# Kernel optimization log

Measured on AMD Instinct MI355X. Metric: run time of the kernel, lower is better.

Reference implementation:

```python
import jax, jax.numpy as jnp
import numpy as np

N = 20000   # nodes
E = 320000  # edges (before self-loops)
D = 256     # feature width (inChl = hdChl = outChl)
H = 4       # heads
C = D // H  # per-head channels = 64
NEG_SLOPE = 0.2
LN_EPS = 1e-5


def setup_inputs() -> dict:
    key = jax.random.key(0)
    ks = jax.random.split(key, 2 + 4 * 4)
    inp = {}
    inp["x"] = jax.random.normal(ks[0], (1, N, D), dtype=jnp.float32)
    inp["edge_index"] = jax.random.randint(ks[1], (2, E), 0, N, dtype=jnp.int32)
    s = 1.0 / np.sqrt(D)
    for i in range(4):
        k = 2 + 4 * i
        inp[f"Wl{i+1}"] = (jax.random.normal(ks[k], (D, H * C), dtype=jnp.float32) * s)
        inp[f"Wr{i+1}"] = (jax.random.normal(ks[k + 1], (D, H * C), dtype=jnp.float32) * s)
        inp[f"att{i+1}"] = (jax.random.normal(ks[k + 2], (H, C), dtype=jnp.float32) * s)
        inp[f"b{i+1}"] = jnp.zeros((H * C,), dtype=jnp.float32)
        inp[f"g{i+1}"] = jnp.ones((D,), dtype=jnp.float32)
        inp[f"be{i+1}"] = jnp.zeros((D,), dtype=jnp.float32)
    return inp


def _segment_softmax(scores, seg, num_segments):
    # scores: [E, H], per-destination softmax over incoming edges
    m = jax.ops.segment_max(scores, seg, num_segments=num_segments)
    e = jnp.exp(scores - m[seg])
    d = jax.ops.segment_sum(e, seg, num_segments=num_segments)
    return e / d[seg]


def _gatv2(x, src, dst, Wl, Wr, att, b):
    # GATv2Conv defaults: share_weights=False, concat=True, negative_slope=0.2
    n = x.shape[0]
    xl = (x @ Wl).reshape(n, H, C)  # source transform
    xr = (x @ Wr).reshape(n, H, C)  # target transform
    m = xl[src] + xr[dst]                                  # [E', H, C]
    e = jnp.sum(jax.nn.leaky_relu(m, NEG_SLOPE) * att, -1) # [E', H]
    alpha = _segment_softmax(e, dst, n)                    # [E', H]
    out = jax.ops.segment_sum(xl[src] * alpha[:, :, None], dst, num_segments=n)
    return out.reshape(n, H * C) + b


def _layernorm(x, g, b):
    mu = jnp.mean(x, -1, keepdims=True)
    var = jnp.mean(jnp.square(x - mu), -1, keepdims=True)
    return (x - mu) * jax.lax.rsqrt(var + LN_EPS) * g + b


def _forward(x, edge_index, layers):
    h = x[0]  # squeeze batch dim -> [N, D]
    n = h.shape[0]
    loop = jnp.arange(n, dtype=edge_index.dtype)
    src = jnp.concatenate([edge_index[0], loop])  # add_self_loops=True
    dst = jnp.concatenate([edge_index[1], loop])
    for (Wl, Wr, att, b, g, be) in layers:
        h = _gatv2(h, src, dst, Wl, Wr, att, b)
        h = jax.nn.relu(_layernorm(h, g, be))
    return h[None]  # unsqueeze -> [1, N, D]


def reference(x, edge_index,
              Wl1, Wr1, att1, b1, g1, be1,
              Wl2, Wr2, att2, b2, g2, be2,
              Wl3, Wr3, att3, b3, g3, be3,
              Wl4, Wr4, att4, b4, g4, be4):
    layers = [(Wl1, Wr1, att1, b1, g1, be1),
              (Wl2, Wr2, att2, b2, g2, be2),
              (Wl3, Wr3, att3, b3, g3, be3),
              (Wl4, Wr4, att4, b4, g4, be4)]
    return _forward(x, edge_index, layers)
```

## Files before the change

### kernel.cpp

```cpp
#include <hip/hip_runtime.h>
#include <math.h>

#define N_NODES 20000
#define E_EDGES 320000
#define EP (E_EDGES + N_NODES)
#define D 256
#define NHEAD 4
#define CH 64
#define NEG_SLOPE 0.2f
#define LN_EPS 1e-5f

typedef _Float16 half8_t __attribute__((ext_vector_type(8)));
typedef _Float16 half4_t __attribute__((ext_vector_type(4)));
typedef _Float16 half2_t __attribute__((ext_vector_type(2)));
typedef float   float4_t __attribute__((ext_vector_type(4)));

__device__ __forceinline__ void async_cp16(const void* g, void* l)
{
    __builtin_amdgcn_global_load_lds(
        (const __attribute__((address_space(1))) void*)g,
        (__attribute__((address_space(3))) void*)l, 16, 0, 0);
}

template<int CTRL>
__device__ __forceinline__ float dpp_add(float v) {
    int t = __builtin_amdgcn_update_dpp(0, __float_as_int(v), CTRL, 0xF, 0xF, true);
    return v + __int_as_float(t);
}
__device__ __forceinline__ float row_sum16(float v) {
    v = dpp_add<0x121>(v);
    v = dpp_add<0x122>(v);
    v = dpp_add<0x124>(v);
    v = dpp_add<0x128>(v);
    return v;
}

__global__ __launch_bounds__(256)
void convert_x_kernel(const float* __restrict__ x, _Float16* __restrict__ h16,
                      int* __restrict__ deg)
{
    int i = blockIdx.x * 256 + threadIdx.x;
    if (i < N_NODES) deg[i] = 0;
    if (i >= N_NODES * D / 4) return;
    float4 v = reinterpret_cast<const float4*>(x)[i];
    half4_t o;
    o.x = (_Float16)v.x; o.y = (_Float16)v.y; o.z = (_Float16)v.z; o.w = (_Float16)v.w;
    reinterpret_cast<half4_t*>(h16)[i] = o;
}

__global__ __launch_bounds__(256)
void csr_hist_kernel(const int* __restrict__ ei, int* __restrict__ deg)
{
    int e = blockIdx.x * 256 + threadIdx.x;
    if (e >= EP) return;
    int dst = (e < E_EDGES) ? ei[E_EDGES + e] : (e - E_EDGES);
    atomicAdd(&deg[dst], 1);
}

__global__ __launch_bounds__(1024)
void csr_scan_kernel(const int* __restrict__ deg, int* __restrict__ rowptr,
                     int* __restrict__ cursor, int* __restrict__ csr_src)
{
    __shared__ int wsum[16];
    int t = threadIdx.x, lane = t & 63, w = t >> 6;
    if (t < 8) csr_src[EP + t] = 0;
    int base = t * 20;
    int loc[20];
    int s = 0;
    #pragma unroll
    for (int k = 0; k < 20; ++k) {
        int idx = base + k;
        loc[k] = (idx < N_NODES) ? deg[idx] : 0;
        s += loc[k];
    }
    int x = s;
    #pragma unroll
    for (int o = 1; o < 64; o <<= 1) {
        int y = __shfl_up(x, o, 64);
        if (lane >= o) x += y;
    }
    if (lane == 63) wsum[w] = x;
    __syncthreads();
    if (t == 0) {
        int sacc = 0;
        #pragma unroll
        for (int k = 0; k < 16; ++k) { int tmp = wsum[k]; wsum[k] = sacc; sacc += tmp; }
        rowptr[N_NODES] = sacc;
    }
    __syncthreads();
    int excl = wsum[w] + x - s;
    #pragma unroll
    for (int k = 0; k < 20; ++k) {
        int idx = base + k;
        if (idx < N_NODES) { rowptr[idx] = excl; cursor[idx] = excl; }
        excl += loc[k];
    }
}

__global__ __launch_bounds__(256)
void csr_scatter_kernel(const int* __restrict__ ei, int* __restrict__ cursor,
                        int* __restrict__ csr_src)
{
    int e = blockIdx.x * 256 + threadIdx.x;
    if (e >= EP) return;
    int src, dst;
    if (e < E_EDGES) { src = ei[e]; dst = ei[E_EDGES + e]; }
    else             { src = dst = e - E_EDGES; }
    int pos = atomicAdd(&cursor[dst], 1);
    csr_src[pos] = src;
}

struct WPtrs { const float* p[8]; };
__global__ __launch_bounds__(256)
void convw_all_kernel(WPtrs wp, _Float16* __restrict__ Wt_all)
{
    __shared__ float tile[64][65];
    const float* W = wp.p[blockIdx.z];
    _Float16* out = Wt_all + (size_t)blockIdx.z * 65536;
    int bx = blockIdx.x * 64, by = blockIdx.y * 64;
    int t = threadIdx.x;
    #pragma unroll
    for (int i = 0; i < 16; ++i) {
        int idx = t + i * 256;
        int kk = idx >> 6, nn = idx & 63;
        tile[kk][nn] = W[(by + kk) * 256 + bx + nn];
    }
    __syncthreads();
    #pragma unroll
    for (int i = 0; i < 16; ++i) {
        int idx = t + i * 256;
        int nn = idx >> 6, kk = idx & 63;
        out[(bx + nn) * 256 + by + kk] = (_Float16)tile[kk][nn];
    }
}

#define BM 128
#define BN 128
#define BK 64
#define EPAD 136
__global__ __launch_bounds__(256)
void gemm_f16_kernel(const _Float16* __restrict__ A16, const _Float16* __restrict__ Wt,
                     _Float16* __restrict__ X0, _Float16* __restrict__ X1, int nrows)
{
    const _Float16* W = Wt + blockIdx.z * 65536 + blockIdx.y * (BN * 256);
    _Float16* X = blockIdx.z ? X1 : X0;
    const int row0 = blockIdx.x * BM;
    const int col0 = blockIdx.y * BN;

    __shared__ __align__(1024) char smem[4 * 32 * EPAD * 2];
    _Float16 (*As)[BK] = reinterpret_cast<_Float16 (*)[BK]>(smem);
    _Float16 (*Bs)[BK] = reinterpret_cast<_Float16 (*)[BK]>(smem + BM * BK * 2);
    _Float16* As_flat = reinterpret_cast<_Float16*>(smem);
    _Float16* Bs_flat = reinterpret_cast<_Float16*>(smem + BM * BK * 2);
    _Float16* ep = reinterpret_cast<_Float16*>(smem);

    const int tid  = threadIdx.x;
    const int wave = tid >> 6, lane = tid & 63;
    const int quad = lane >> 4, l16 = lane & 15;

    float4_t acc[2][8];
    #pragma unroll
    for (int i = 0; i < 2; ++i)
        #pragma unroll
        for (int j = 0; j < 8; ++j) acc[i][j] = (float4_t)0.0f;

    const int r_in  = lane >> 3;
    const int c_in  = (lane & 7) * 8;

    #pragma unroll
    for (int k0 = 0; k0 < 256; k0 += BK) {
        #pragma unroll
        for (int j = 0; j < 4; ++j) {
            int ia  = wave * 4 + j;
            int row = ia * 8 + r_in;
            int gra = row0 + row;
            gra = (gra < nrows) ? gra : (nrows - 1);
            async_cp16(A16 + (size_t)gra * 256 + k0 + c_in, As_flat + ia * 512);
            async_cp16(W   + (size_t)row * 256 + k0 + c_in, Bs_flat + ia * 512);
        }
        __syncthreads();

        #pragma unroll
        for (int s = 0; s < 2; ++s) {
            half8_t af[2], bf[8];
            #pragma unroll
            for (int i = 0; i < 2; ++i)
                af[i] = *reinterpret_cast<const half8_t*>(&As[wave * 32 + i * 16 + l16][s * 32 + quad * 8]);
            #pragma unroll
            for (int j = 0; j < 8; ++j)
                bf[j] = *reinterpret_cast<const half8_t*>(&Bs[j * 16 + l16][s * 32 + quad * 8]);
            #pragma unroll
            for (int i = 0; i < 2; ++i)
                #pragma unroll
                for (int j = 0; j < 8; ++j)
                    acc[i][j] = __builtin_amdgcn_mfma_f32_16x16x32_f16(af[i], bf[j], acc[i][j], 0, 0, 0);
        }
        __syncthreads();
    }

    _Float16* epw = ep + wave * 32 * EPAD;
    #pragma unroll
    for (int i = 0; i < 2; ++i)
        #pragma unroll
        for (int j = 0; j < 8; ++j)
            #pragma unroll
            for (int r = 0; r < 4; ++r)
                epw[(i * 16 + quad * 4 + r) * EPAD + j * 16 + l16] = (_Float16)acc[i][j][r];
    #pragma unroll
    for (int t = 0; t < 8; ++t) {
        int row = t * 4 + quad;
        int gr = row0 + wave * 32 + row;
        half8_t v = *reinterpret_cast<const half8_t*>(&epw[row * EPAD + l16 * 8]);
        if (gr < nrows)
            *reinterpret_cast<half8_t*>(X + gr * 256 + col0 + l16 * 8) = v;
    }
}

__global__ __launch_bounds__(256)
void gat_fused_kernel(const _Float16* __restrict__ xl, const _Float16* __restrict__ xr,
                      const int* __restrict__ rowptr, const int* __restrict__ csr_src,
                      const float* __restrict__ att,
                      const float* __restrict__ bias, const float* __restrict__ g,
                      const float* __restrict__ be,
                      float* __restrict__ out32, _Float16* __restrict__ out16,
                      int write32)
{
    const int tid = threadIdx.x;
    const int w = tid >> 6, lane = tid & 63;
    const int n = blockIdx.x * 4 + w;
    const int start = rowptr[n], end = rowptr[n + 1];
    const int c0 = lane * 4;

    half2_t xr01, xr23, att01, att23;
    {
        half4_t xh = *reinterpret_cast<const half4_t*>(xr + n * D + c0);
        xr01.x = xh.x; xr01.y = xh.y; xr23.x = xh.z; xr23.y = xh.w;
        float4 av = *reinterpret_cast<const float4*>(att + c0);
        att01.x = (_Float16)av.x; att01.y = (_Float16)av.y;
        att23.x = (_Float16)av.z; att23.y = (_Float16)av.w;
    }
    const half2_t k02 = {(_Float16)NEG_SLOPE, (_Float16)NEG_SLOPE};

    float den = 0.0f;
    float4 num = make_float4(0.0f, 0.0f, 0.0f, 0.0f);

    int i = start;
    for (; i + 8 <= end; i += 8) {
        int sidx[8];
        #pragma unroll
        for (int j = 0; j < 8; ++j) sidx[j] = csr_src[i + j];
        half4_t h[8];
        #pragma unroll
        for (int j = 0; j < 8; ++j)
            h[j] = *reinterpret_cast<const half4_t*>(xl + sidx[j] * D + c0);
        float p[8];
        #pragma unroll
        for (int j = 0; j < 8; ++j) {
            half2_t a01 = {h[j].x, h[j].y}, a23 = {h[j].z, h[j].w};
            half2_t t0 = a01 + xr01, t1 = a23 + xr23;
            t0 = __builtin_elementwise_max(t0, t0 * k02);
            t1 = __builtin_elementwise_max(t1, t1 * k02);
            float v = __builtin_amdgcn_fdot2(t0, att01, 0.0f, false);
            p[j]    = __builtin_amdgcn_fdot2(t1, att23, v,   false);
        }
        #pragma unroll
        for (int j = 0; j < 8; ++j) p[j] = row_sum16(p[j]);
        #pragma unroll
        for (int j = 0; j < 8; ++j) p[j] = __expf(p[j]);
        #pragma unroll
        for (int j = 0; j < 8; ++j) {
            den += p[j];
            num.x = fmaf(p[j], (float)h[j].x, num.x);
            num.y = fmaf(p[j], (float)h[j].y, num.y);
            num.z = fmaf(p[j], (float)h[j].z, num.z);
            num.w = fmaf(p[j], (float)h[j].w, num.w);
        }
    }
    for (; i < end; i += 4) {
        int sidx[4];
        #pragma unroll
        for (int j = 0; j < 4; ++j) sidx[j] = csr_src[i + j];
        half4_t h[4];
        #pragma unroll
        for (int j = 0; j < 4; ++j)
            h[j] = *reinterpret_cast<const half4_t*>(xl + sidx[j] * D + c0);
        float p[4];
        #pragma unroll
        for (int j = 0; j < 4; ++j) {
            half2_t a01 = {h[j].x, h[j].y}, a23 = {h[j].z, h[j].w};
            half2_t t0 = a01 + xr01, t1 = a23 + xr23;
            t0 = __builtin_elementwise_max(t0, t0 * k02);
            t1 = __builtin_elementwise_max(t1, t1 * k02);
            float v = __builtin_amdgcn_fdot2(t0, att01, 0.0f, false);
            p[j]    = __builtin_amdgcn_fdot2(t1, att23, v,   false);
        }
        #pragma unroll
        for (int j = 0; j < 4; ++j) p[j] = row_sum16(p[j]);
        #pragma unroll
        for (int j = 0; j < 4; ++j) {
            float pj = (i + j < end) ? __expf(p[j]) : 0.0f;
            den += pj;
            num.x = fmaf(pj, (float)h[j].x, num.x);
            num.y = fmaf(pj, (float)h[j].y, num.y);
            num.z = fmaf(pj, (float)h[j].z, num.z);
            num.w = fmaf(pj, (float)h[j].w, num.w);
        }
    }

    float inv_den = 1.0f / den;
    float4 bi = *reinterpret_cast<const float4*>(bias + c0);
    float a0 = fmaf(num.x, inv_den, bi.x);
    float a1 = fmaf(num.y, inv_den, bi.y);
    float a2 = fmaf(num.z, inv_den, bi.z);
    float a3 = fmaf(num.w, inv_den, bi.w);

    float wsum = a0 + a1 + a2 + a3;
    float wsq  = a0 * a0 + a1 * a1 + a2 * a2 + a3 * a3;
    #pragma unroll
    for (int o = 1; o < 64; o <<= 1) {
        wsum += __shfl_xor(wsum, o, 64);
        wsq  += __shfl_xor(wsq,  o, 64);
    }
    float mu = wsum * (1.0f / 256.0f);
    float var = wsq * (1.0f / 256.0f) - mu * mu;
    float rstd = rsqrtf(var + LN_EPS);

    float4 gg = *reinterpret_cast<const float4*>(g + c0);
    float4 bb = *reinterpret_cast<const float4*>(be + c0);
    float o0 = fmaxf((a0 - mu) * rstd * gg.x + bb.x, 0.0f);
    float o1 = fmaxf((a1 - mu) * rstd * gg.y + bb.y, 0.0f);
    float o2 = fmaxf((a2 - mu) * rstd * gg.z + bb.z, 0.0f);
    float o3 = fmaxf((a3 - mu) * rstd * gg.w + bb.w, 0.0f);

    if (write32) {
        float4 o4 = make_float4(o0, o1, o2, o3);
        *reinterpret_cast<float4*>(out32 + n * D + c0) = o4;
    } else {
        half4_t o4;
        o4.x = (_Float16)o0; o4.y = (_Float16)o1; o4.z = (_Float16)o2; o4.w = (_Float16)o3;
        *reinterpret_cast<half4_t*>(out16 + n * D + c0) = o4;
    }
}

extern "C" void kernel_launch(void* const* d_in, const int* in_sizes, int n_in,
                              void* d_out, int out_size, void* d_ws, size_t ws_size,
                              hipStream_t stream)
{
    const float* x  = (const float*)d_in[0];
    const int*   ei = (const int*)d_in[1];

    char* ws = (char*)d_ws;
    size_t off = 0;
    _Float16* h16   = (_Float16*)(ws + off); off += (size_t)N_NODES * D * 2;
    _Float16* xl    = (_Float16*)(ws + off); off += (size_t)N_NODES * D * 2;
    _Float16* xr    = (_Float16*)(ws + off); off += (size_t)N_NODES * D * 2;
    _Float16* WtA   = (_Float16*)(ws + off); off += (size_t)8 * 65536 * 2;
    int* rowptr     = (int*)(ws + off);      off += (size_t)(N_NODES + 32) * 4;
    int* cursor     = (int*)(ws + off);      off += (size_t)N_NODES * 4;
    int* csr_src    = (int*)(ws + off);      off += (size_t)(EP + 32) * 4;

    convert_x_kernel<<<(N_NODES * D / 4 + 255) / 256, 256, 0, stream>>>(x, h16, cursor);
    csr_hist_kernel<<<(EP + 255) / 256, 256, 0, stream>>>(ei, cursor);
    csr_scan_kernel<<<1, 1024, 0, stream>>>(cursor, rowptr, cursor, csr_src);
    csr_scatter_kernel<<<(EP + 255) / 256, 256, 0, stream>>>(ei, cursor, csr_src);

    WPtrs wp;
    for (int l = 0; l < 4; ++l) {
        wp.p[2 * l + 0] = (const float*)d_in[2 + 6 * l + 0];
        wp.p[2 * l + 1] = (const float*)d_in[2 + 6 * l + 1];
    }
    convw_all_kernel<<<dim3(4, 4, 8), 256, 0, stream>>>(wp, WtA);

    dim3 gemm_grid((N_NODES + BM - 1) / BM, 256 / BN, 2);

    for (int l = 0; l < 4; ++l) {
        const float* att  = (const float*)d_in[2 + 6 * l + 2];
        const float* bias = (const float*)d_in[2 + 6 * l + 3];
        const float* g    = (const float*)d_in[2 + 6 * l + 4];
        const float* be   = (const float*)d_in[2 + 6 * l + 5];

        gemm_f16_kernel<<<gemm_grid, 256, 0, stream>>>(h16, WtA + (size_t)l * 131072,
                                                       xl, xr, N_NODES);
        gat_fused_kernel<<<N_NODES / 4, 256, 0, stream>>>(xl, xr, rowptr, csr_src, att,
                                                          bias, g, be,
                                                          (float*)d_out, h16, (l == 3) ? 1 : 0);
    }
}
```

Measured before the change: 355.6 us.

## Fuse degree histogram into conversion kernel and double GEMM row tile

Merges the edge-degree histogram into the fp32-to-fp16 conversion kernel, replacing the in-kernel degree zeroing with a memset, which removes one launch. It also raises the GEMM M tile from 128 to 256 rows so each wave computes 64 rows, reusing each B tile across more rows at the cost of a larger accumulator set and more LDS. The epilogue is split into two halves so the existing per-wave staging buffer still fits. The larger tile halves the number of GEMM blocks, which may reduce occupancy and CU load balance on a 20000-row problem.

```diff
diff --git a/kernel.cpp b/kernel.cpp
--- a/kernel.cpp
+++ b/kernel.cpp
@@ -36,25 +36,19 @@
 }
 
 __global__ __launch_bounds__(256)
-void convert_x_kernel(const float* __restrict__ x, _Float16* __restrict__ h16,
-                      int* __restrict__ deg)
+void convert_hist_kernel(const float* __restrict__ x, _Float16* __restrict__ h16,
+                         const int* __restrict__ ei, int* __restrict__ deg)
 {
     int i = blockIdx.x * 256 + threadIdx.x;
-    if (i < N_NODES) deg[i] = 0;
+    if (i < EP) {
+        int dst = (i < E_EDGES) ? ei[E_EDGES + i] : (i - E_EDGES);
+        atomicAdd(&deg[dst], 1);
+    }
     if (i >= N_NODES * D / 4) return;
     float4 v = reinterpret_cast<const float4*>(x)[i];
     half4_t o;
     o.x = (_Float16)v.x; o.y = (_Float16)v.y; o.z = (_Float16)v.z; o.w = (_Float16)v.w;
     reinterpret_cast<half4_t*>(h16)[i] = o;
-}
-
-__global__ __launch_bounds__(256)
-void csr_hist_kernel(const int* __restrict__ ei, int* __restrict__ deg)
-{
-    int e = blockIdx.x * 256 + threadIdx.x;
-    if (e >= EP) return;
-    int dst = (e < E_EDGES) ? ei[E_EDGES + e] : (e - E_EDGES);
-    atomicAdd(&deg[dst], 1);
 }
 
 __global__ __launch_bounds__(1024)
@@ -134,7 +128,7 @@
     }
 }
 
-#define BM 128
+#define BM 256
 #define BN 128
 #define BK 64
 #define EPAD 136
@@ -147,7 +141,7 @@
     const int row0 = blockIdx.x * BM;
     const int col0 = blockIdx.y * BN;
 
-    __shared__ __align__(1024) char smem[4 * 32 * EPAD * 2];
+    __shared__ __align__(1024) char smem[BM * BK * 2 + BN * BK * 2];
     _Float16 (*As)[BK] = reinterpret_cast<_Float16 (*)[BK]>(smem);
     _Float16 (*Bs)[BK] = reinterpret_cast<_Float16 (*)[BK]>(smem + BM * BK * 2);
     _Float16* As_flat = reinterpret_cast<_Float16*>(smem);
@@ -158,9 +152,9 @@
     const int wave = tid >> 6, lane = tid & 63;
     const int quad = lane >> 4, l16 = lane & 15;
 
-    float4_t acc[2][8];
-    #pragma unroll
-    for (int i = 0; i < 2; ++i)
+    float4_t acc[4][8];
+    #pragma unroll
+    for (int i = 0; i < 4; ++i)
         #pragma unroll
         for (int j = 0; j < 8; ++j) acc[i][j] = (float4_t)0.0f;
 
@@ -170,27 +164,32 @@
     #pragma unroll
     for (int k0 = 0; k0 < 256; k0 += BK) {
         #pragma unroll
-        for (int j = 0; j < 4; ++j) {
-            int ia  = wave * 4 + j;
+        for (int j = 0; j < 8; ++j) {
+            int ia  = wave * 8 + j;
             int row = ia * 8 + r_in;
             int gra = row0 + row;
             gra = (gra < nrows) ? gra : (nrows - 1);
             async_cp16(A16 + (size_t)gra * 256 + k0 + c_in, As_flat + ia * 512);
-            async_cp16(W   + (size_t)row * 256 + k0 + c_in, Bs_flat + ia * 512);
+        }
+        #pragma unroll
+        for (int j = 0; j < 4; ++j) {
+            int ib  = wave * 4 + j;
+            int row = ib * 8 + r_in;
+            async_cp16(W + (size_t)row * 256 + k0 + c_in, Bs_flat + ib * 512);
         }
         __syncthreads();
 
         #pragma unroll
         for (int s = 0; s < 2; ++s) {
-            half8_t af[2], bf[8];
+            half8_t af[4], bf[8];
             #pragma unroll
-            for (int i = 0; i < 2; ++i)
-                af[i] = *reinterpret_cast<const half8_t*>(&As[wave * 32 + i * 16 + l16][s * 32 + quad * 8]);
+            for (int i = 0; i < 4; ++i)
+                af[i] = *reinterpret_cast<const half8_t*>(&As[wave * 64 + i * 16 + l16][s * 32 + quad * 8]);
             #pragma unroll
             for (int j = 0; j < 8; ++j)
                 bf[j] = *reinterpret_cast<const half8_t*>(&Bs[j * 16 + l16][s * 32 + quad * 8]);
             #pragma unroll
-            for (int i = 0; i < 2; ++i)
+            for (int i = 0; i < 4; ++i)
                 #pragma unroll
                 for (int j = 0; j < 8; ++j)
                     acc[i][j] = __builtin_amdgcn_mfma_f32_16x16x32_f16(af[i], bf[j], acc[i][j], 0, 0, 0);
@@ -200,19 +199,24 @@
 
     _Float16* epw = ep + wave * 32 * EPAD;
     #pragma unroll
-    for (int i = 0; i < 2; ++i)
-        #pragma unroll
-        for (int j = 0; j < 8; ++j)
+    for (int c = 0; c < 2; ++c) {
+        #pragma unroll
+        for (int ii = 0; ii < 2; ++ii) {
+            int itile = c * 2 + ii;
             #pragma unroll
-            for (int r = 0; r < 4; ++r)
-                epw[(i * 16 + quad * 4 + r) * EPAD + j * 16 + l16] = (_Float16)acc[i][j][r];
-    #pragma unroll
-    for (int t = 0; t < 8; ++t) {
-        int row = t * 4 + quad;
-        int gr = row0 + wave * 32 + row;
-        half8_t v = *reinterpret_cast<const half8_t*>(&epw[row * EPAD + l16 * 8]);
-        if (gr < nrows)
-            *reinterpret_cast<half8_t*>(X + gr * 256 + col0 + l16 * 8) = v;
+            for (int j = 0; j < 8; ++j)
+                #pragma unroll
+                for (int r = 0; r < 4; ++r)
+                    epw[(ii * 16 + quad * 4 + r) * EPAD + j * 16 + l16] = (_Float16)acc[itile][j][r];
+        }
+        #pragma unroll
+        for (int t = 0; t < 8; ++t) {
+            int row = t * 4 + quad;
+            int gr = row0 + wave * 64 + c * 32 + row;
+            half8_t v = *reinterpret_cast<const half8_t*>(&epw[row * EPAD + l16 * 8]);
+            if (gr < nrows)
+                *reinterpret_cast<half8_t*>(X + gr * 256 + col0 + l16 * 8) = v;
+        }
     }
 }
 
@@ -359,8 +363,8 @@
     int* cursor     = (int*)(ws + off);      off += (size_t)N_NODES * 4;
     int* csr_src    = (int*)(ws + off);      off += (size_t)(EP + 32) * 4;
 
-    convert_x_kernel<<<(N_NODES * D / 4 + 255) / 256, 256, 0, stream>>>(x, h16, cursor);
-    csr_hist_kernel<<<(EP + 255) / 256, 256, 0, stream>>>(ei, cursor);
+    hipMemsetAsync(cursor, 0, (size_t)N_NODES * 4, stream);
+    convert_hist_kernel<<<(N_NODES * D / 4 + 255) / 256, 256, 0, stream>>>(x, h16, ei, cursor);
     csr_scan_kernel<<<1, 1024, 0, stream>>>(cursor, rowptr, cursor, csr_src);
     csr_scatter_kernel<<<(EP + 255) / 256, 256, 0, stream>>>(ei, cursor, csr_src);
 
```

Result: slower. 386.8 us (+8.8%).
